# Optimization experiments

Measured on AMD Instinct MI355X. Metric: run time of the kernel, lower is better.

## Reference

```python
import jax, jax.numpy as jnp
import numpy as np

# DynamicMaskHead config (CondLaneHead defaults, head_layers=3, channels=64)
N, INS_PER_IMG, C, H, W = 4, 8, 64, 160, 256
CIN = C + 2  # coords concatenated
L1, L2, L3 = (C + 2) * C, C * C, C * 1  # weight_nums = [4224, 4096, 64]
B1, B2, B3 = C, C, 1                     # bias_nums   = [64, 64, 1]
NUM_PARAMS = L1 + L2 + L3 + B1 + B2 + B3  # 8513
MASK_BIAS_SHIFT = 2.19  # subtracted from last bias when is_mask=True


def setup_inputs() -> dict:
    key = jax.random.key(0)
    k1, k2 = jax.random.split(key)
    x = jax.random.normal(k1, (N, C, H, W), dtype=jnp.float32)
    mask_head_params = jax.random.normal(k2, (N * INS_PER_IMG, NUM_PARAMS), dtype=jnp.float32) * 0.05
    num_ins = np.full((N,), INS_PER_IMG, dtype=np.int32)  # static per-image instance counts
    return {"x": x, "mask_head_params": mask_head_params, "num_ins": num_ins}


def _locations(h, w, dtype):
    # compute_locations with stride=1: +stride//2 == +0; original normalization
    # (locations[:0], locations[:1]) is a no-op slice, so coords stay unnormalized.
    loc_x = jnp.broadcast_to(jnp.arange(w, dtype=dtype)[None, :], (h, w))
    loc_y = jnp.broadcast_to(jnp.arange(h, dtype=dtype)[:, None], (h, w))
    return jnp.stack([loc_x, loc_y], axis=0)  # [2, H, W]


def reference(x, mask_head_params, num_ins):
    n, _, h, w = x.shape
    loc = _locations(h, w, x.dtype)
    xa = jnp.concatenate([jnp.broadcast_to(loc[None], (n, 2, h, w)), x], axis=1)  # [N, 66, H, W]

    # replicate each image's features per instance (grouped-conv input)
    img_idx = np.repeat(np.arange(n), np.asarray(num_ins))  # static
    num_insts = img_idx.shape[0]
    feats = xa[img_idx].reshape(num_insts, CIN, h * w)  # [I, 66, L]

    # parse_dynamic_params: split flat params into per-instance 1x1 conv weights/biases
    splits = jnp.split(mask_head_params, np.cumsum([L1, L2, L3, B1, B2]), axis=1)
    w0 = splits[0].reshape(num_insts, C, CIN)
    w1 = splits[1].reshape(num_insts, C, C)
    w2 = splits[2].reshape(num_insts, 1, C)
    b0 = splits[3]
    b1 = splits[4]
    b2 = splits[5] - MASK_BIAS_SHIFT  # is_mask=True

    # grouped 1x1 convs == per-instance small matmuls (batched GEMM)
    hdn = jax.nn.relu(jnp.einsum('ioc,icl->iol', w0, feats) + b0[:, :, None])
    hdn = jax.nn.relu(jnp.einsum('ioc,icl->iol', w1, hdn) + b1[:, :, None])
    out = jnp.einsum('ioc,icl->iol', w2, hdn) + b2[:, :, None]  # [I, 1, L]
    return out.reshape(1, num_insts, h, w)
```

## Files before the change

kernel.cpp:

```cpp
#include <hip/hip_runtime.h>
#include <hip/hip_bf16.h>


#define NP 8513
#define HW 40960
#define WSI 20480

typedef __attribute__((ext_vector_type(8))) short bf16x8;
typedef __attribute__((ext_vector_type(4))) float f32x4;

__device__ inline unsigned short f2bf(float f) {
  union { float f; unsigned u; } v; v.f = f;
  unsigned r = v.u + 0x7fffu + ((v.u >> 16) & 1u);
  return (unsigned short)(r >> 16);
}
__device__ inline unsigned pk2(float a, float b) {
  __hip_bfloat162 h = __float22bfloat162_rn(float2{a, b});
  union { __hip_bfloat162 h; unsigned u; } v; v.h = h;
  return v.u;
}

__global__ void condlane_prep(const float* __restrict__ params,
                              char* __restrict__ ws) {
  const int inst = blockIdx.x >> 3, part = blockIdx.x & 7;
  const float* __restrict__ p = params + inst * NP;
  char* base = ws + inst * WSI;
  const int t = threadIdx.x;
  if (part < 2) {
    unsigned short* dst = (unsigned short*)base;
#pragma unroll
    for (int it = 0; it < 8; it++) {
      const int e = part * 2048 + it * 256 + t;
      const int frag = e >> 9, lane = (e >> 3) & 63, j = e & 7;
      const int m = (frag >> 1) * 16 + (lane & 15);
      const int k = (frag & 1) * 32 + ((lane >> 4) << 3) + j;
      dst[e] = f2bf(p[m * 66 + 2 + k]);
    }
  } else if (part < 4) {
    unsigned short* dst = (unsigned short*)(base + 8192);
#pragma unroll
    for (int it = 0; it < 8; it++) {
      const int e = (part - 2) * 2048 + it * 256 + t;
      const int frag = e >> 9, lane = (e >> 3) & 63, j = e & 7;
      const int m = (frag >> 1) * 16 + (lane & 15);
      const int k = (frag & 1) * 32 + ((lane >> 4) << 3) + j;
      dst[e] = f2bf(p[4224 + m * 64 + k]);
    }
  } else if (part == 4) {
    float* vec = (float*)(base + 16384);
    if (t < 64) {
      vec[t]       = p[8384 + t];
      vec[64 + t]  = p[t * 66];
      vec[128 + t] = p[t * 66 + 1];
      vec[192 + t] = p[8448 + t];
      vec[256 + t] = p[8320 + t];
    } else if (t == 64) vec[320] = p[8512] - 2.19f;
    for (int e = 321 + t; e < 1024; e += 256) vec[e] = 0.f;
  }
}

__global__ __launch_bounds__(256, 2) void condlane_main(
    const float* __restrict__ x, const char* __restrict__ ws,
    float* __restrict__ out) {
  __shared__ __align__(16) unsigned short xs[256 * 64];
  __shared__ __align__(16) char wl[2][WSI];
  const int img = blockIdx.y, bx = blockIdx.x;
  const int tid = threadIdx.x, lane = tid & 63, wave = tid >> 6;
  const int col = lane & 15, q = lane >> 4;

  {
    const float* gx = x + img * 64 * HW + bx * 256 + tid;
    unsigned short* row = xs + tid * 64;
    const int psw = tid & 7;
#pragma unroll
    for (int cb = 0; cb < 8; cb++) {
      union { bf16x8 v; unsigned short s[8]; } u;
#pragma unroll
      for (int j = 0; j < 8; j++) u.s[j] = f2bf(gx[(cb * 8 + j) * HW]);
      *(bf16x8*)(row + ((cb ^ psw) << 3)) = u.v;
    }
  }
  const char* wsi = ws + img * 8 * WSI;
  {
    uint4 st[5];
#pragma unroll
    for (int j = 0; j < 5; j++)
      st[j] = *(const uint4*)(wsi + j * 4096 + tid * 16);
#pragma unroll
    for (int j = 0; j < 5; j++)
      *(uint4*)(wl[0] + j * 4096 + tid * 16) = st[j];
  }
  __syncthreads();

  bf16x8 bfr[4][2];
#pragma unroll
  for (int nt = 0; nt < 4; nt++)
#pragma unroll
    for (int ks = 0; ks < 2; ks++) {
      const int row = wave * 64 + nt * 16 + col;
      bfr[nt][ks] = *(const bf16x8*)(xs + row * 64 +
                                     (((ks * 4 + q) ^ (row & 7)) << 3));
    }
  const float fyv = (float)bx;
  float fxv[4];
#pragma unroll
  for (int nt = 0; nt < 4; nt++) fxv[nt] = (float)(wave * 64 + nt * 16 + col);

  const int srcA = ((lane >> 4) & 1) * 32 + col;
  const int srcB = srcA + 16;
  const bool lowq = q < 2;
  float* outb = out + img * 8 * HW + bx * 256 + wave * 64 + lane;

  for (int i = 0; i < 8; i++) {
    uint4 st[5];
    if (i < 7) {
#pragma unroll
      for (int j = 0; j < 5; j++)
        st[j] = *(const uint4*)(wsi + (i + 1) * WSI + j * 4096 + tid * 16);
    }
    const char* lb = wl[i & 1];
    const unsigned short* w0f = (const unsigned short*)lb;
    const unsigned short* w1f = (const unsigned short*)(lb + 8192);
    const float* vec = (const float*)(lb + 16384);

    f32x4 acc[4][4];
#pragma unroll
    for (int mt = 0; mt < 4; mt++) {
      const int ro = mt * 16 + q * 4;
      const f32x4 b0v = *(const f32x4*)(vec + ro);
      const f32x4 wxv = *(const f32x4*)(vec + 64 + ro);
      const f32x4 wyv = *(const f32x4*)(vec + 128 + ro);
      const f32x4 byv = b0v + wyv * fyv;
#pragma unroll
      for (int nt = 0; nt < 4; nt++) acc[mt][nt] = byv + wxv * fxv[nt];
    }
#pragma unroll
    for (int mt = 0; mt < 4; mt++) {
      const bf16x8 a0 = *(const bf16x8*)(w0f + (mt * 2 + 0) * 512 + lane * 8);
      const bf16x8 a1 = *(const bf16x8*)(w0f + (mt * 2 + 1) * 512 + lane * 8);
#pragma unroll
      for (int nt = 0; nt < 4; nt++) {
        f32x4 c = __builtin_amdgcn_mfma_f32_16x16x32_bf16(a0, bfr[nt][0],
                                                          acc[mt][nt], 0, 0, 0);
        acc[mt][nt] = __builtin_amdgcn_mfma_f32_16x16x32_bf16(a1, bfr[nt][1],
                                                              c, 0, 0, 0);
      }
    }
    unsigned pk0[4][4], pk1[4][4];
#pragma unroll
    for (int mt = 0; mt < 4; mt++)
#pragma unroll
      for (int nt = 0; nt < 4; nt++) {
        const f32x4 v = acc[mt][nt];
        pk0[mt][nt] = pk2(fmaxf(v.x, 0.f), fmaxf(v.y, 0.f));
        pk1[mt][nt] = pk2(fmaxf(v.z, 0.f), fmaxf(v.w, 0.f));
      }
    bf16x8 hbf[4][2];
#pragma unroll
    for (int nt = 0; nt < 4; nt++)
#pragma unroll
      for (int ks = 0; ks < 2; ks++) {
        const int mA = 2 * ks, mB = 2 * ks + 1;
        const unsigned tA0 = __shfl((int)pk0[mA][nt], srcA, 64);
        const unsigned tA1 = __shfl((int)pk1[mA][nt], srcA, 64);
        const unsigned tA2 = __shfl((int)pk0[mA][nt], srcB, 64);
        const unsigned tA3 = __shfl((int)pk1[mA][nt], srcB, 64);
        const unsigned tB0 = __shfl((int)pk0[mB][nt], srcA, 64);
        const unsigned tB1 = __shfl((int)pk1[mB][nt], srcA, 64);
        const unsigned tB2 = __shfl((int)pk0[mB][nt], srcB, 64);
        const unsigned tB3 = __shfl((int)pk1[mB][nt], srcB, 64);
        union { bf16x8 v; unsigned d[4]; } u;
        u.d[0] = lowq ? tA0 : tB0;
        u.d[1] = lowq ? tA1 : tB1;
        u.d[2] = lowq ? tA2 : tB2;
        u.d[3] = lowq ? tA3 : tB3;
        hbf[nt][ks] = u.v;
      }
    float s[4] = {0.f, 0.f, 0.f, 0.f};
#pragma unroll
    for (int mt = 0; mt < 4; mt++) {
      const int ro = mt * 16 + q * 4;
      const f32x4 cb  = *(const f32x4*)(vec + 192 + ro);
      const f32x4 w2v = *(const f32x4*)(vec + 256 + ro);
      const bf16x8 a0 = *(const bf16x8*)(w1f + (mt * 2 + 0) * 512 + lane * 8);
      const bf16x8 a1 = *(const bf16x8*)(w1f + (mt * 2 + 1) * 512 + lane * 8);
#pragma unroll
      for (int nt = 0; nt < 4; nt++) {
        f32x4 c = __builtin_amdgcn_mfma_f32_16x16x32_bf16(a0, hbf[nt][0],
                                                          cb, 0, 0, 0);
        const f32x4 v = __builtin_amdgcn_mfma_f32_16x16x32_bf16(a1, hbf[nt][1],
                                                                c, 0, 0, 0);
        s[nt] += w2v.x * fmaxf(v.x, 0.f) + w2v.y * fmaxf(v.y, 0.f) +
                 w2v.z * fmaxf(v.z, 0.f) + w2v.w * fmaxf(v.w, 0.f);
      }
    }
    const float b2 = vec[320];
#pragma unroll
    for (int nt = 0; nt < 4; nt++) {
      s[nt] += __shfl_xor(s[nt], 16, 64);
      s[nt] += __shfl_xor(s[nt], 32, 64);
    }
    const float sel = (q == 0) ? s[0] : (q == 1) ? s[1] : (q == 2) ? s[2] : s[3];
    outb[i * HW] = sel + b2;

    if (i < 7) {
      char* nb = wl[(i + 1) & 1];
#pragma unroll
      for (int j = 0; j < 5; j++)
        *(uint4*)(nb + j * 4096 + tid * 16) = st[j];
      __syncthreads();
    }
  }
}

extern "C" void kernel_launch(void* const* d_in, const int* in_sizes, int n_in,
                              void* d_out, int out_size, void* d_ws, size_t ws_size,
                              hipStream_t stream) {
  const float* x      = (const float*)d_in[0];
  const float* params = (const float*)d_in[1];
  float* out = (float*)d_out;

  condlane_prep<<<256, 256, 0, stream>>>(params, (char*)d_ws);
  condlane_main<<<dim3(160, 4), 256, 0, stream>>>(x, (const char*)d_ws, out);
}
```

Baseline: 131.2 us.

## Fold coord/bias terms into an extra MFMA and shrink LDS for higher occupancy

The coordinate weights and first-layer bias move into a third K-slice of the layer-0 weight fragments, with hi/lo bf16 splits for precision, and are multiplied by an augmented B operand holding [1, x, x, y, y, 1]. This replaces the per-iteration FMA initialisation of the accumulators. The layer-1 input transpose now goes through an LDS scratch region instead of many cross-lane shuffles. The weight buffer is single-buffered and aliased over the x staging area, which cuts LDS and allows launch bounds of 3 blocks per CU. The cost is extra barriers per instance and one more MFMA per tile, and the prep kernel is consolidated from 256 blocks to 64.

```diff
diff --git a/kernel.cpp b/kernel.cpp
--- a/kernel.cpp
+++ b/kernel.cpp
@@ -4,7 +4,9 @@
 
 #define NP 8513
 #define HW 40960
-#define WSI 20480
+#define ISTRIDE 21504
+#define OFF_W1 12288
+#define OFF_VEC 20480
 
 typedef __attribute__((ext_vector_type(8))) short bf16x8;
 typedef __attribute__((ext_vector_type(4))) float f32x4;
@@ -14,6 +16,10 @@
   unsigned r = v.u + 0x7fffu + ((v.u >> 16) & 1u);
   return (unsigned short)(r >> 16);
 }
+__device__ inline float bf2f(unsigned short b) {
+  union { unsigned u; float f; } v; v.u = ((unsigned)b) << 16;
+  return v.f;
+}
 __device__ inline unsigned pk2(float a, float b) {
   __hip_bfloat162 h = __float22bfloat162_rn(float2{a, b});
   union { __hip_bfloat162 h; unsigned u; } v; v.h = h;
@@ -22,51 +28,61 @@
 
 __global__ void condlane_prep(const float* __restrict__ params,
                               char* __restrict__ ws) {
-  const int inst = blockIdx.x >> 3, part = blockIdx.x & 7;
+  const int inst = blockIdx.x >> 1, part = blockIdx.x & 1;
   const float* __restrict__ p = params + inst * NP;
-  char* base = ws + inst * WSI;
-  const int t = threadIdx.x;
-  if (part < 2) {
+  char* base = ws + inst * ISTRIDE;
+  if (part == 0) {
     unsigned short* dst = (unsigned short*)base;
 #pragma unroll
-    for (int it = 0; it < 8; it++) {
-      const int e = part * 2048 + it * 256 + t;
+    for (int it = 0; it < 24; it++) {
+      const int e = it * 256 + threadIdx.x;
       const int frag = e >> 9, lane = (e >> 3) & 63, j = e & 7;
-      const int m = (frag >> 1) * 16 + (lane & 15);
-      const int k = (frag & 1) * 32 + ((lane >> 4) << 3) + j;
-      dst[e] = f2bf(p[m * 66 + 2 + k]);
-    }
-  } else if (part < 4) {
-    unsigned short* dst = (unsigned short*)(base + 8192);
-#pragma unroll
-    for (int it = 0; it < 8; it++) {
-      const int e = (part - 2) * 2048 + it * 256 + t;
+      const int mt = frag / 3, kst = frag % 3;
+      const int m = mt * 16 + (lane & 15);
+      const int kl = ((lane >> 4) << 3) + j;
+      unsigned short bv;
+      if (kst < 2) bv = f2bf(p[m * 66 + 2 + kst * 32 + kl]);
+      else if (kl == 0) bv = f2bf(p[8384 + m]);
+      else if (kl == 1) bv = f2bf(p[m * 66]);
+      else if (kl == 2) { float w = p[m * 66];     bv = f2bf(w - bf2f(f2bf(w))); }
+      else if (kl == 3) bv = f2bf(p[m * 66 + 1]);
+      else if (kl == 4) { float w = p[m * 66 + 1]; bv = f2bf(w - bf2f(f2bf(w))); }
+      else if (kl == 5) { float w = p[8384 + m];   bv = f2bf(w - bf2f(f2bf(w))); }
+      else bv = 0;
+      dst[e] = bv;
+    }
+  } else {
+    unsigned short* dst = (unsigned short*)(base + OFF_W1);
+#pragma unroll
+    for (int it = 0; it < 16; it++) {
+      const int e = it * 256 + threadIdx.x;
       const int frag = e >> 9, lane = (e >> 3) & 63, j = e & 7;
       const int m = (frag >> 1) * 16 + (lane & 15);
       const int k = (frag & 1) * 32 + ((lane >> 4) << 3) + j;
       dst[e] = f2bf(p[4224 + m * 64 + k]);
     }
-  } else if (part == 4) {
-    float* vec = (float*)(base + 16384);
-    if (t < 64) {
-      vec[t]       = p[8384 + t];
-      vec[64 + t]  = p[t * 66];
-      vec[128 + t] = p[t * 66 + 1];
-      vec[192 + t] = p[8448 + t];
-      vec[256 + t] = p[8320 + t];
-    } else if (t == 64) vec[320] = p[8512] - 2.19f;
-    for (int e = 321 + t; e < 1024; e += 256) vec[e] = 0.f;
-  }
-}
-
-__global__ __launch_bounds__(256, 2) void condlane_main(
+    float* vec = (float*)(base + OFF_VEC);
+    const int t = threadIdx.x;
+    if (t < 64) { vec[t] = p[8448 + t]; vec[64 + t] = p[8320 + t]; }
+    else if (t == 64) vec[128] = p[8512] - 2.19f;
+  }
+}
+
+__global__ __launch_bounds__(256, 3) void condlane_main(
     const float* __restrict__ x, const char* __restrict__ ws,
     float* __restrict__ out) {
-  __shared__ __align__(16) unsigned short xs[256 * 64];
-  __shared__ __align__(16) char wl[2][WSI];
+  __shared__ __align__(16) char smem[37888];
+  unsigned short* const xs = (unsigned short*)smem;
+  char* const wl = smem;
   const int img = blockIdx.y, bx = blockIdx.x;
   const int tid = threadIdx.x, lane = tid & 63, wave = tid >> 6;
-  const int col = lane & 15, q = lane >> 4;
+  const int col = lane & 15, q = lane >> 4, sw = lane & 7;
+  const char* const wsb = ws + img * 8 * ISTRIDE;
+
+  uint4 st[6];
+#pragma unroll
+  for (int j = 0; j < 6; j++)
+    if (j < 5 || tid < 64) st[j] = *(const uint4*)(wsb + j * 4096 + tid * 16);
 
   {
     const float* gx = x + img * 64 * HW + bx * 256 + tid;
@@ -80,16 +96,6 @@
       *(bf16x8*)(row + ((cb ^ psw) << 3)) = u.v;
     }
   }
-  const char* wsi = ws + img * 8 * WSI;
-  {
-    uint4 st[5];
-#pragma unroll
-    for (int j = 0; j < 5; j++)
-      st[j] = *(const uint4*)(wsi + j * 4096 + tid * 16);
-#pragma unroll
-    for (int j = 0; j < 5; j++)
-      *(uint4*)(wl[0] + j * 4096 + tid * 16) = st[j];
-  }
   __syncthreads();
 
   bf16x8 bfr[4][2];
@@ -101,100 +107,93 @@
       bfr[nt][ks] = *(const bf16x8*)(xs + row * 64 +
                                      (((ks * 4 + q) ^ (row & 7)) << 3));
     }
-  const float fyv = (float)bx;
-  float fxv[4];
-#pragma unroll
-  for (int nt = 0; nt < 4; nt++) fxv[nt] = (float)(wave * 64 + nt * 16 + col);
-
-  const int srcA = ((lane >> 4) & 1) * 32 + col;
-  const int srcB = srcA + 16;
-  const bool lowq = q < 2;
-  float* outb = out + img * 8 * HW + bx * 256 + wave * 64 + lane;
+  bf16x8 baug[4];
+  {
+    const unsigned short fyb = f2bf((float)bx);
+#pragma unroll
+    for (int nt = 0; nt < 4; nt++) {
+      const unsigned short fxb = f2bf((float)(wave * 64 + nt * 16 + col));
+      union { bf16x8 v; unsigned short s[8]; } u;
+      u.s[0] = (q == 0) ? (unsigned short)0x3F80 : (unsigned short)0;
+      u.s[1] = (q == 0) ? fxb : (unsigned short)0;
+      u.s[2] = u.s[1];
+      u.s[3] = (q == 0) ? fyb : (unsigned short)0;
+      u.s[4] = u.s[3];
+      u.s[5] = u.s[0];
+      u.s[6] = 0; u.s[7] = 0;
+      baug[nt] = u.v;
+    }
+  }
+  __syncthreads();
+
+#pragma unroll
+  for (int j = 0; j < 6; j++)
+    if (j < 5 || tid < 64) *(uint4*)(wl + j * 4096 + tid * 16) = st[j];
+  __syncthreads();
+
+  unsigned short* const hw = (unsigned short*)(smem + 21504) + wave * 2048;
+  const f32x4 z4 = {0.f, 0.f, 0.f, 0.f};
+  float* const outb = out + img * 8 * HW + bx * 256 + wave * 64 + lane;
 
   for (int i = 0; i < 8; i++) {
-    uint4 st[5];
     if (i < 7) {
-#pragma unroll
-      for (int j = 0; j < 5; j++)
-        st[j] = *(const uint4*)(wsi + (i + 1) * WSI + j * 4096 + tid * 16);
-    }
-    const char* lb = wl[i & 1];
-    const unsigned short* w0f = (const unsigned short*)lb;
-    const unsigned short* w1f = (const unsigned short*)(lb + 8192);
-    const float* vec = (const float*)(lb + 16384);
-
+      const char* src = wsb + (i + 1) * ISTRIDE;
+#pragma unroll
+      for (int j = 0; j < 6; j++)
+        if (j < 5 || tid < 64) st[j] = *(const uint4*)(src + j * 4096 + tid * 16);
+    }
     f32x4 acc[4][4];
 #pragma unroll
     for (int mt = 0; mt < 4; mt++) {
+      const bf16x8 a0 = *(const bf16x8*)(wl + (mt * 3 + 0) * 1024 + lane * 16);
+      const bf16x8 a1 = *(const bf16x8*)(wl + (mt * 3 + 1) * 1024 + lane * 16);
+      const bf16x8 a2 = *(const bf16x8*)(wl + (mt * 3 + 2) * 1024 + lane * 16);
+#pragma unroll
+      for (int nt = 0; nt < 4; nt++) {
+        f32x4 c = __builtin_amdgcn_mfma_f32_16x16x32_bf16(a0, bfr[nt][0], z4, 0, 0, 0);
+        c = __builtin_amdgcn_mfma_f32_16x16x32_bf16(a1, bfr[nt][1], c, 0, 0, 0);
+        acc[mt][nt] = __builtin_amdgcn_mfma_f32_16x16x32_bf16(a2, baug[nt], c, 0, 0, 0);
+      }
+    }
+    bf16x8 hbf[4][2];
+#pragma unroll
+    for (int hh = 0; hh < 2; hh++) {
+#pragma unroll
+      for (int mt = 0; mt < 4; mt++)
+#pragma unroll
+        for (int ntl = 0; ntl < 2; ntl++) {
+          const f32x4 v = acc[mt][hh * 2 + ntl];
+          uint2 dd;
+          dd.x = pk2(fmaxf(v.x, 0.f), fmaxf(v.y, 0.f));
+          dd.y = pk2(fmaxf(v.z, 0.f), fmaxf(v.w, 0.f));
+          const int kb = (mt * 2 + (q >> 1)) ^ sw;
+          *(uint2*)(hw + (ntl * 16 + col) * 64 + (kb << 3) + ((q & 1) << 2)) = dd;
+        }
+#pragma unroll
+      for (int ntl = 0; ntl < 2; ntl++)
+#pragma unroll
+        for (int ks = 0; ks < 2; ks++)
+          hbf[hh * 2 + ntl][ks] = *(const bf16x8*)(hw + (ntl * 16 + col) * 64 +
+                                                   (((ks * 4 + q) ^ sw) << 3));
+    }
+    const float* vecf = (const float*)(wl + OFF_VEC);
+    float s[4] = {0.f, 0.f, 0.f, 0.f};
+#pragma unroll
+    for (int mt = 0; mt < 4; mt++) {
+      const bf16x8 a0 = *(const bf16x8*)(wl + OFF_W1 + (mt * 2 + 0) * 1024 + lane * 16);
+      const bf16x8 a1 = *(const bf16x8*)(wl + OFF_W1 + (mt * 2 + 1) * 1024 + lane * 16);
       const int ro = mt * 16 + q * 4;
-      const f32x4 b0v = *(const f32x4*)(vec + ro);
-      const f32x4 wxv = *(const f32x4*)(vec + 64 + ro);
-      const f32x4 wyv = *(const f32x4*)(vec + 128 + ro);
-      const f32x4 byv = b0v + wyv * fyv;
-#pragma unroll
-      for (int nt = 0; nt < 4; nt++) acc[mt][nt] = byv + wxv * fxv[nt];
-    }
-#pragma unroll
-    for (int mt = 0; mt < 4; mt++) {
-      const bf16x8 a0 = *(const bf16x8*)(w0f + (mt * 2 + 0) * 512 + lane * 8);
-      const bf16x8 a1 = *(const bf16x8*)(w0f + (mt * 2 + 1) * 512 + lane * 8);
+      const f32x4 cb  = *(const f32x4*)(vecf + ro);
+      const f32x4 w2v = *(const f32x4*)(vecf + 64 + ro);
 #pragma unroll
       for (int nt = 0; nt < 4; nt++) {
-        f32x4 c = __builtin_amdgcn_mfma_f32_16x16x32_bf16(a0, bfr[nt][0],
-                                                          acc[mt][nt], 0, 0, 0);
-        acc[mt][nt] = __builtin_amdgcn_mfma_f32_16x16x32_bf16(a1, bfr[nt][1],
-                                                              c, 0, 0, 0);
-      }
-    }
-    unsigned pk0[4][4], pk1[4][4];
-#pragma unroll
-    for (int mt = 0; mt < 4; mt++)
-#pragma unroll
-      for (int nt = 0; nt < 4; nt++) {
-        const f32x4 v = acc[mt][nt];
-        pk0[mt][nt] = pk2(fmaxf(v.x, 0.f), fmaxf(v.y, 0.f));
-        pk1[mt][nt] = pk2(fmaxf(v.z, 0.f), fmaxf(v.w, 0.f));
-      }
-    bf16x8 hbf[4][2];
-#pragma unroll
-    for (int nt = 0; nt < 4; nt++)
-#pragma unroll
-      for (int ks = 0; ks < 2; ks++) {
-        const int mA = 2 * ks, mB = 2 * ks + 1;
-        const unsigned tA0 = __shfl((int)pk0[mA][nt], srcA, 64);
-        const unsigned tA1 = __shfl((int)pk1[mA][nt], srcA, 64);
-        const unsigned tA2 = __shfl((int)pk0[mA][nt], srcB, 64);
-        const unsigned tA3 = __shfl((int)pk1[mA][nt], srcB, 64);
-        const unsigned tB0 = __shfl((int)pk0[mB][nt], srcA, 64);
-        const unsigned tB1 = __shfl((int)pk1[mB][nt], srcA, 64);
-        const unsigned tB2 = __shfl((int)pk0[mB][nt], srcB, 64);
-        const unsigned tB3 = __shfl((int)pk1[mB][nt], srcB, 64);
-        union { bf16x8 v; unsigned d[4]; } u;
-        u.d[0] = lowq ? tA0 : tB0;
-        u.d[1] = lowq ? tA1 : tB1;
-        u.d[2] = lowq ? tA2 : tB2;
-        u.d[3] = lowq ? tA3 : tB3;
-        hbf[nt][ks] = u.v;
-      }
-    float s[4] = {0.f, 0.f, 0.f, 0.f};
-#pragma unroll
-    for (int mt = 0; mt < 4; mt++) {
-      const int ro = mt * 16 + q * 4;
-      const f32x4 cb  = *(const f32x4*)(vec + 192 + ro);
-      const f32x4 w2v = *(const f32x4*)(vec + 256 + ro);
-      const bf16x8 a0 = *(const bf16x8*)(w1f + (mt * 2 + 0) * 512 + lane * 8);
-      const bf16x8 a1 = *(const bf16x8*)(w1f + (mt * 2 + 1) * 512 + lane * 8);
-#pragma unroll
-      for (int nt = 0; nt < 4; nt++) {
-        f32x4 c = __builtin_amdgcn_mfma_f32_16x16x32_bf16(a0, hbf[nt][0],
-                                                          cb, 0, 0, 0);
-        const f32x4 v = __builtin_amdgcn_mfma_f32_16x16x32_bf16(a1, hbf[nt][1],
-                                                                c, 0, 0, 0);
+        f32x4 c = __builtin_amdgcn_mfma_f32_16x16x32_bf16(a0, hbf[nt][0], cb, 0, 0, 0);
+        const f32x4 v = __builtin_amdgcn_mfma_f32_16x16x32_bf16(a1, hbf[nt][1], c, 0, 0, 0);
         s[nt] += w2v.x * fmaxf(v.x, 0.f) + w2v.y * fmaxf(v.y, 0.f) +
                  w2v.z * fmaxf(v.z, 0.f) + w2v.w * fmaxf(v.w, 0.f);
       }
     }
-    const float b2 = vec[320];
+    const float b2 = vecf[128];
 #pragma unroll
     for (int nt = 0; nt < 4; nt++) {
       s[nt] += __shfl_xor(s[nt], 16, 64);
@@ -204,10 +203,10 @@
     outb[i * HW] = sel + b2;
 
     if (i < 7) {
-      char* nb = wl[(i + 1) & 1];
-#pragma unroll
-      for (int j = 0; j < 5; j++)
-        *(uint4*)(nb + j * 4096 + tid * 16) = st[j];
+      __syncthreads();
+#pragma unroll
+      for (int j = 0; j < 6; j++)
+        if (j < 5 || tid < 64) *(uint4*)(wl + j * 4096 + tid * 16) = st[j];
       __syncthreads();
     }
   }
@@ -220,6 +219,6 @@
   const float* params = (const float*)d_in[1];
   float* out = (float*)d_out;
 
-  condlane_prep<<<256, 256, 0, stream>>>(params, (char*)d_ws);
+  condlane_prep<<<64, 256, 0, stream>>>(params, (char*)d_ws);
   condlane_main<<<dim3(160, 4), 256, 0, stream>>>(x, (const char*)d_ws, out);
 }
```

Result: slower. 144.7 us (+10.2%).

## Halve pixel tile, single-buffer weights, and pass hidden activations through LDS

Applied to the files above, without the earlier changes.

Each block now handles 128 pixels instead of 256, so the grid doubles to 320x4. The x tile is loaded straight into MFMA B-fragment registers rather than staged through LDS. Weights are single-buffered in a smaller LDS region with a tighter workspace stride, and layer-1 outputs move to layer-2 inputs through a swizzled per-wave LDS scratch instead of many cross-lane shuffles. Launch bounds rise to 5 blocks per CU to increase occupancy and cut shuffle and LDS pressure. In exchange it adds an extra barrier per instance and makes the weight reloads less overlapped with compute.

```diff
diff --git a/kernel.cpp b/kernel.cpp
--- a/kernel.cpp
+++ b/kernel.cpp
@@ -4,7 +4,9 @@
 
 #define NP 8513
 #define HW 40960
-#define WSI 20480
+#define ISTRIDE 17920
+#define OFF_W1 8192
+#define OFF_VEC 16384
 
 typedef __attribute__((ext_vector_type(8))) short bf16x8;
 typedef __attribute__((ext_vector_type(4))) float f32x4;
@@ -22,32 +24,31 @@
 
 __global__ void condlane_prep(const float* __restrict__ params,
                               char* __restrict__ ws) {
-  const int inst = blockIdx.x >> 3, part = blockIdx.x & 7;
+  const int inst = blockIdx.x >> 1, part = blockIdx.x & 1;
   const float* __restrict__ p = params + inst * NP;
-  char* base = ws + inst * WSI;
+  char* base = ws + inst * ISTRIDE;
   const int t = threadIdx.x;
-  if (part < 2) {
+  if (part == 0) {
     unsigned short* dst = (unsigned short*)base;
 #pragma unroll
-    for (int it = 0; it < 8; it++) {
-      const int e = part * 2048 + it * 256 + t;
+    for (int it = 0; it < 16; it++) {
+      const int e = it * 256 + t;
       const int frag = e >> 9, lane = (e >> 3) & 63, j = e & 7;
       const int m = (frag >> 1) * 16 + (lane & 15);
       const int k = (frag & 1) * 32 + ((lane >> 4) << 3) + j;
       dst[e] = f2bf(p[m * 66 + 2 + k]);
     }
-  } else if (part < 4) {
-    unsigned short* dst = (unsigned short*)(base + 8192);
+  } else {
+    unsigned short* dst = (unsigned short*)(base + OFF_W1);
 #pragma unroll
-    for (int it = 0; it < 8; it++) {
-      const int e = (part - 2) * 2048 + it * 256 + t;
+    for (int it = 0; it < 16; it++) {
+      const int e = it * 256 + t;
       const int frag = e >> 9, lane = (e >> 3) & 63, j = e & 7;
       const int m = (frag >> 1) * 16 + (lane & 15);
       const int k = (frag & 1) * 32 + ((lane >> 4) << 3) + j;
       dst[e] = f2bf(p[4224 + m * 64 + k]);
     }
-  } else if (part == 4) {
-    float* vec = (float*)(base + 16384);
+    float* vec = (float*)(base + OFF_VEC);
     if (t < 64) {
       vec[t]       = p[8384 + t];
       vec[64 + t]  = p[t * 66];
@@ -55,75 +56,64 @@
       vec[192 + t] = p[8448 + t];
       vec[256 + t] = p[8320 + t];
     } else if (t == 64) vec[320] = p[8512] - 2.19f;
-    for (int e = 321 + t; e < 1024; e += 256) vec[e] = 0.f;
+    if (t >= 65 && t < 128) vec[256 + t] = 0.f;
   }
 }
 
-__global__ __launch_bounds__(256, 2) void condlane_main(
+__global__ __launch_bounds__(256, 5) void condlane_main(
     const float* __restrict__ x, const char* __restrict__ ws,
     float* __restrict__ out) {
-  __shared__ __align__(16) unsigned short xs[256 * 64];
-  __shared__ __align__(16) char wl[2][WSI];
+  __shared__ __align__(16) char smem[26112];
+  char* const wl = smem;
+  const float* const vec = (const float*)(smem + OFF_VEC);
   const int img = blockIdx.y, bx = blockIdx.x;
   const int tid = threadIdx.x, lane = tid & 63, wave = tid >> 6;
-  const int col = lane & 15, q = lane >> 4;
+  const int col = lane & 15, q = lane >> 4, sw = col & 7;
+  const char* const wsb = ws + img * 8 * ISTRIDE;
 
+  uint4 st[4]; uint4 stv;
   {
-    const float* gx = x + img * 64 * HW + bx * 256 + tid;
-    unsigned short* row = xs + tid * 64;
-    const int psw = tid & 7;
 #pragma unroll
-    for (int cb = 0; cb < 8; cb++) {
-      union { bf16x8 v; unsigned short s[8]; } u;
+    for (int j = 0; j < 4; j++) st[j] = *(const uint4*)(wsb + j * 4096 + tid * 16);
+    if (tid < 96) stv = *(const uint4*)(wsb + OFF_VEC + tid * 16);
+  }
+  bf16x8 bfr[2][2];
+  {
+    const float* gx = x + img * 64 * HW + bx * 128 + wave * 32;
 #pragma unroll
-      for (int j = 0; j < 8; j++) u.s[j] = f2bf(gx[(cb * 8 + j) * HW]);
-      *(bf16x8*)(row + ((cb ^ psw) << 3)) = u.v;
-    }
+    for (int nt = 0; nt < 2; nt++)
+#pragma unroll
+      for (int ks = 0; ks < 2; ks++) {
+        float f[8];
+#pragma unroll
+        for (int j = 0; j < 8; j++)
+          f[j] = gx[(ks * 32 + q * 8 + j) * HW + nt * 16 + col];
+        union { bf16x8 v; unsigned d[4]; } u;
+#pragma unroll
+        for (int jj = 0; jj < 4; jj++) u.d[jj] = pk2(f[2 * jj], f[2 * jj + 1]);
+        bfr[nt][ks] = u.v;
+      }
   }
-  const char* wsi = ws + img * 8 * WSI;
-  {
-    uint4 st[5];
 #pragma unroll
-    for (int j = 0; j < 5; j++)
-      st[j] = *(const uint4*)(wsi + j * 4096 + tid * 16);
-#pragma unroll
-    for (int j = 0; j < 5; j++)
-      *(uint4*)(wl[0] + j * 4096 + tid * 16) = st[j];
-  }
+  for (int j = 0; j < 4; j++) *(uint4*)(wl + j * 4096 + tid * 16) = st[j];
+  if (tid < 96) *(uint4*)(smem + OFF_VEC + tid * 16) = stv;
   __syncthreads();
 
-  bf16x8 bfr[4][2];
-#pragma unroll
-  for (int nt = 0; nt < 4; nt++)
-#pragma unroll
-    for (int ks = 0; ks < 2; ks++) {
-      const int row = wave * 64 + nt * 16 + col;
-      bfr[nt][ks] = *(const bf16x8*)(xs + row * 64 +
-                                     (((ks * 4 + q) ^ (row & 7)) << 3));
-    }
-  const float fyv = (float)bx;
-  float fxv[4];
-#pragma unroll
-  for (int nt = 0; nt < 4; nt++) fxv[nt] = (float)(wave * 64 + nt * 16 + col);
-
-  const int srcA = ((lane >> 4) & 1) * 32 + col;
-  const int srcB = srcA + 16;
-  const bool lowq = q < 2;
-  float* outb = out + img * 8 * HW + bx * 256 + wave * 64 + lane;
+  const float fyv = (float)(bx >> 1);
+  const float fx0 = (float)((bx & 1) * 128 + wave * 32 + col);
+  unsigned short* const hwv = (unsigned short*)(smem + 17920) + wave * 1024;
+  float* const outb = out + img * 8 * HW + bx * 128 + wave * 32;
 
   for (int i = 0; i < 8; i++) {
-    uint4 st[5];
     if (i < 7) {
+      const char* src = wsb + (i + 1) * ISTRIDE;
 #pragma unroll
-      for (int j = 0; j < 5; j++)
-        st[j] = *(const uint4*)(wsi + (i + 1) * WSI + j * 4096 + tid * 16);
+      for (int j = 0; j < 4; j++) st[j] = *(const uint4*)(src + j * 4096 + tid * 16);
+      if (tid < 96) stv = *(const uint4*)(src + OFF_VEC + tid * 16);
     }
-    const char* lb = wl[i & 1];
-    const unsigned short* w0f = (const unsigned short*)lb;
-    const unsigned short* w1f = (const unsigned short*)(lb + 8192);
-    const float* vec = (const float*)(lb + 16384);
+    const float b2i = vec[320];
 
-    f32x4 acc[4][4];
+    f32x4 acc[4][2];
 #pragma unroll
     for (int mt = 0; mt < 4; mt++) {
       const int ro = mt * 16 + q * 4;
@@ -131,83 +121,64 @@
       const f32x4 wxv = *(const f32x4*)(vec + 64 + ro);
       const f32x4 wyv = *(const f32x4*)(vec + 128 + ro);
       const f32x4 byv = b0v + wyv * fyv;
-#pragma unroll
-      for (int nt = 0; nt < 4; nt++) acc[mt][nt] = byv + wxv * fxv[nt];
+      acc[mt][0] = byv + wxv * fx0;
+      acc[mt][1] = byv + wxv * (fx0 + 16.0f);
     }
 #pragma unroll
     for (int mt = 0; mt < 4; mt++) {
-      const bf16x8 a0 = *(const bf16x8*)(w0f + (mt * 2 + 0) * 512 + lane * 8);
-      const bf16x8 a1 = *(const bf16x8*)(w0f + (mt * 2 + 1) * 512 + lane * 8);
+      const bf16x8 a0 = *(const bf16x8*)(wl + (mt * 2 + 0) * 1024 + lane * 16);
+      const bf16x8 a1 = *(const bf16x8*)(wl + (mt * 2 + 1) * 1024 + lane * 16);
 #pragma unroll
-      for (int nt = 0; nt < 4; nt++) {
+      for (int nt = 0; nt < 2; nt++) {
         f32x4 c = __builtin_amdgcn_mfma_f32_16x16x32_bf16(a0, bfr[nt][0],
                                                           acc[mt][nt], 0, 0, 0);
         acc[mt][nt] = __builtin_amdgcn_mfma_f32_16x16x32_bf16(a1, bfr[nt][1],
                                                               c, 0, 0, 0);
       }
     }
-    unsigned pk0[4][4], pk1[4][4];
+    bf16x8 hbf[2][2];
 #pragma unroll
-    for (int mt = 0; mt < 4; mt++)
+    for (int nt = 0; nt < 2; nt++) {
 #pragma unroll
-      for (int nt = 0; nt < 4; nt++) {
+      for (int mt = 0; mt < 4; mt++) {
         const f32x4 v = acc[mt][nt];
-        pk0[mt][nt] = pk2(fmaxf(v.x, 0.f), fmaxf(v.y, 0.f));
-        pk1[mt][nt] = pk2(fmaxf(v.z, 0.f), fmaxf(v.w, 0.f));
+        uint2 dd;
+        dd.x = pk2(fmaxf(v.x, 0.f), fmaxf(v.y, 0.f));
+        dd.y = pk2(fmaxf(v.z, 0.f), fmaxf(v.w, 0.f));
+        const int kb = (mt * 2 + (q >> 1)) ^ sw;
+        *(uint2*)(hwv + col * 64 + (kb << 3) + ((q & 1) << 2)) = dd;
       }
-    bf16x8 hbf[4][2];
 #pragma unroll
-    for (int nt = 0; nt < 4; nt++)
-#pragma unroll
-      for (int ks = 0; ks < 2; ks++) {
-        const int mA = 2 * ks, mB = 2 * ks + 1;
-        const unsigned tA0 = __shfl((int)pk0[mA][nt], srcA, 64);
-        const unsigned tA1 = __shfl((int)pk1[mA][nt], srcA, 64);
-        const unsigned tA2 = __shfl((int)pk0[mA][nt], srcB, 64);
-        const unsigned tA3 = __shfl((int)pk1[mA][nt], srcB, 64);
-        const unsigned tB0 = __shfl((int)pk0[mB][nt], srcA, 64);
-        const unsigned tB1 = __shfl((int)pk1[mB][nt], srcA, 64);
-        const unsigned tB2 = __shfl((int)pk0[mB][nt], srcB, 64);
-        const unsigned tB3 = __shfl((int)pk1[mB][nt], srcB, 64);
-        union { bf16x8 v; unsigned d[4]; } u;
-        u.d[0] = lowq ? tA0 : tB0;
-        u.d[1] = lowq ? tA1 : tB1;
-        u.d[2] = lowq ? tA2 : tB2;
-        u.d[3] = lowq ? tA3 : tB3;
-        hbf[nt][ks] = u.v;
-      }
-    float s[4] = {0.f, 0.f, 0.f, 0.f};
+      for (int ks = 0; ks < 2; ks++)
+        hbf[nt][ks] = *(const bf16x8*)(hwv + col * 64 + (((ks * 4 + q) ^ sw) << 3));
+    }
+    float s0 = 0.f, s1 = 0.f;
 #pragma unroll
     for (int mt = 0; mt < 4; mt++) {
+      const bf16x8 a0 = *(const bf16x8*)(wl + OFF_W1 + (mt * 2 + 0) * 1024 + lane * 16);
+      const bf16x8 a1 = *(const bf16x8*)(wl + OFF_W1 + (mt * 2 + 1) * 1024 + lane * 16);
       const int ro = mt * 16 + q * 4;
       const f32x4 cb  = *(const f32x4*)(vec + 192 + ro);
       const f32x4 w2v = *(const f32x4*)(vec + 256 + ro);
-      const bf16x8 a0 = *(const bf16x8*)(w1f + (mt * 2 + 0) * 512 + lane * 8);
-      const bf16x8 a1 = *(const bf16x8*)(w1f + (mt * 2 + 1) * 512 + lane * 8);
-#pragma unroll
-      for (int nt = 0; nt < 4; nt++) {
-        f32x4 c = __builtin_amdgcn_mfma_f32_16x16x32_bf16(a0, hbf[nt][0],
-                                                          cb, 0, 0, 0);
-        const f32x4 v = __builtin_amdgcn_mfma_f32_16x16x32_bf16(a1, hbf[nt][1],
-                                                                c, 0, 0, 0);
-        s[nt] += w2v.x * fmaxf(v.x, 0.f) + w2v.y * fmaxf(v.y, 0.f) +
-                 w2v.z * fmaxf(v.z, 0.f) + w2v.w * fmaxf(v.w, 0.f);
-      }
+      f32x4 c0 = __builtin_amdgcn_mfma_f32_16x16x32_bf16(a0, hbf[0][0], cb, 0, 0, 0);
+      const f32x4 v0 = __builtin_amdgcn_mfma_f32_16x16x32_bf16(a1, hbf[0][1], c0, 0, 0, 0);
+      f32x4 c1 = __builtin_amdgcn_mfma_f32_16x16x32_bf16(a0, hbf[1][0], cb, 0, 0, 0);
+      const f32x4 v1 = __builtin_amdgcn_mfma_f32_16x16x32_bf16(a1, hbf[1][1], c1, 0, 0, 0);
+      s0 += w2v.x * fmaxf(v0.x, 0.f) + w2v.y * fmaxf(v0.y, 0.f) +
+            w2v.z * fmaxf(v0.z, 0.f) + w2v.w * fmaxf(v0.w, 0.f);
+      s1 += w2v.x * fmaxf(v1.x, 0.f) + w2v.y * fmaxf(v1.y, 0.f) +
+            w2v.z * fmaxf(v1.z, 0.f) + w2v.w * fmaxf(v1.w, 0.f);
     }
-    const float b2 = vec[320];
-#pragma unroll
-    for (int nt = 0; nt < 4; nt++) {
-      s[nt] += __shfl_xor(s[nt], 16, 64);
-      s[nt] += __shfl_xor(s[nt], 32, 64);
-    }
-    const float sel = (q == 0) ? s[0] : (q == 1) ? s[1] : (q == 2) ? s[2] : s[3];
-    outb[i * HW] = sel + b2;
+    s0 += __shfl_xor(s0, 16, 64); s0 += __shfl_xor(s0, 32, 64);
+    s1 += __shfl_xor(s1, 16, 64); s1 += __shfl_xor(s1, 32, 64);
+    if (lane < 32)
+      outb[i * HW + q * 16 + col] = (q ? s1 : s0) + b2i;
 
     if (i < 7) {
-      char* nb = wl[(i + 1) & 1];
+      __syncthreads();
 #pragma unroll
-      for (int j = 0; j < 5; j++)
-        *(uint4*)(nb + j * 4096 + tid * 16) = st[j];
+      for (int j = 0; j < 4; j++) *(uint4*)(wl + j * 4096 + tid * 16) = st[j];
+      if (tid < 96) *(uint4*)(smem + OFF_VEC + tid * 16) = stv;
       __syncthreads();
     }
   }
@@ -220,6 +191,6 @@
   const float* params = (const float*)d_in[1];
   float* out = (float*)d_out;
 
-  condlane_prep<<<256, 256, 0, stream>>>(params, (char*)d_ws);
-  condlane_main<<<dim3(160, 4), 256, 0, stream>>>(x, (const char*)d_ws, out);
+  condlane_prep<<<64, 256, 0, stream>>>(params, (char*)d_ws);
+  condlane_main<<<dim3(320, 4), 256, 0, stream>>>(x, (const char*)d_ws, out);
 }
```

New measurement: 141.9 us. +8.1%, slower.
